# Kernel optimization log

Hardware: AMD Instinct MI355X
Metric: run time of the kernel (lower is better)

Reference implementation:

```python
import jax, jax.numpy as jnp
import numpy as np

OUT_H, OUT_W = 7, 7
SPATIAL_SCALE = 1.0  # aligned=True (align_corners=True interpolate), per init_kwargs


def setup_inputs() -> dict:
    key = jax.random.key(0)
    kf, kb, kx, ky, kw, kh = jax.random.split(key, 6)
    B, C, H, W = 4, 256, 200, 200
    N = 512
    features = jax.random.normal(kf, (B, C, H, W), dtype=jnp.float32)
    batch_idx = jax.random.randint(kb, (N,), 0, B, dtype=jnp.int32)
    # integer boxes with x2>x1, y2>y1, strictly inside the map
    x1 = jax.random.randint(kx, (N,), 0, W - 64, dtype=jnp.int32)
    y1 = jax.random.randint(ky, (N,), 0, H - 64, dtype=jnp.int32)
    bw = jax.random.randint(kw, (N,), 8, 64, dtype=jnp.int32)
    bh = jax.random.randint(kh, (N,), 8, 64, dtype=jnp.int32)
    x2 = jnp.minimum(x1 + bw, W - 1)
    y2 = jnp.minimum(y1 + bh, H - 1)
    rois = jnp.stack([batch_idx, x1, y1, x2, y2], axis=1)  # [N, 5] int32
    return {"features": features, "rois": rois}


def reference(features, rois):
    # features: [B, C, H, W]; rois: [N, 5] int32 (batch, x1, y1, x2, y2)
    # Faithful to: crop features[b, :, y1:y2+1, x1:x2+1] then
    # F.interpolate(size=(7,7), mode='bilinear', align_corners=True).
    N = rois.shape[0]
    H, W = features.shape[2], features.shape[3]
    b = rois[:, 0]
    coords = rois[:, 1:5].astype(jnp.float32) * SPATIAL_SCALE
    x1, y1, x2, y2 = coords[:, 0], coords[:, 1], coords[:, 2], coords[:, 3]

    # align_corners=True source coords inside the crop, offset into the full map
    jy = jnp.arange(OUT_H, dtype=jnp.float32)
    jx = jnp.arange(OUT_W, dtype=jnp.float32)
    sy = y1[:, None] + jy[None, :] * (y2 - y1)[:, None] / (OUT_H - 1)  # [N, OH]
    sx = x1[:, None] + jx[None, :] * (x2 - x1)[:, None] / (OUT_W - 1)  # [N, OW]

    y0f = jnp.floor(sy); x0f = jnp.floor(sx)
    wy = sy - y0f                                  # [N, OH]
    wx = sx - x0f                                  # [N, OW]
    y0 = jnp.clip(y0f.astype(jnp.int32), 0, H - 1)
    y1i = jnp.clip(y0 + 1, 0, H - 1)
    x0 = jnp.clip(x0f.astype(jnp.int32), 0, W - 1)
    x1i = jnp.clip(x0 + 1, 0, W - 1)

    bb = b[:, None, None]                          # [N,1,1]

    def gather(yi, xi):
        # advanced indexing -> [N, OH, OW, C]
        return features[bb, :, yi[:, :, None], xi[:, None, :]]

    v00 = gather(y0, x0)
    v01 = gather(y0, x1i)
    v10 = gather(y1i, x0)
    v11 = gather(y1i, x1i)

    wyb = wy[:, :, None, None]                     # [N, OH, 1, 1]
    wxb = wx[:, None, :, None]                     # [N, 1, OW, 1]
    out = (v00 * (1 - wyb) * (1 - wxb) + v01 * (1 - wyb) * wxb
           + v10 * wyb * (1 - wxb) + v11 * wyb * wxb)  # [N, OH, OW, C]
    return jnp.transpose(out, (0, 3, 1, 2))        # [N, C, OH, OW]
```

## Files before the change

kernel.cpp:

```cpp
#include <hip/hip_runtime.h>
#include <hip/hip_bf16.h>
#include <string.h>

#define OUT_H 7
#define OUT_W 7
#define FEAT_H 200
#define FEAT_W 200
#define HW_ALL (FEAT_H * FEAT_W)
#define HWB  32
#define LSTR 260

__device__ inline unsigned pack2_bf16(float a, float b) {
    __hip_bfloat16 ha = __float2bfloat16(a);
    __hip_bfloat16 hb = __float2bfloat16(b);
    unsigned short ua, ub;
    memcpy(&ua, &ha, 2);
    memcpy(&ub, &hb, 2);
    return (unsigned)ua | ((unsigned)ub << 16);
}

__global__ __launch_bounds__(256) void nchw_to_nhwc_bf16_v2(
    const float* __restrict__ in,
    unsigned*    __restrict__ outu,
    int HW)
{
    __shared__ float tile[HWB * LSTR];
    int hw0 = blockIdx.x * HWB;
    int b   = blockIdx.y;
    const float* inb = in + (size_t)b * 256 * HW + hw0;

    int lane = threadIdx.x & 63;
    int w    = threadIdx.x >> 6;
    int cg   = lane >> 3;
    int xq   = lane & 7;
    int hwr  = xq << 2;

#pragma unroll
    for (int cc = 0; cc < 8; ++cc) {
        int c = (w << 6) + (cc << 3) + cg;
        float4 v = *(const float4*)(inb + (size_t)c * HW + hwr);
        tile[(hwr + 0) * LSTR + c] = v.x;
        tile[(hwr + 1) * LSTR + c] = v.y;
        tile[(hwr + 2) * LSTR + c] = v.z;
        tile[(hwr + 3) * LSTR + c] = v.w;
    }
    __syncthreads();

    uint2* ob = (uint2*)outu + ((size_t)b * HW + hw0) * 64;
    int t = threadIdx.x;
#pragma unroll
    for (int i = 0; i < 8; ++i) {
        int q2  = (i << 8) + t;
        int hr  = q2 >> 6;
        int c0  = (q2 & 63) << 2;
        float4 v = *(const float4*)&tile[hr * LSTR + c0];
        uint2 o;
        o.x = pack2_bf16(v.x, v.y);
        o.y = pack2_bf16(v.z, v.w);
        ob[q2] = o;
    }
}

__global__ __launch_bounds__(256) void roialign_nhwc_v3(
    const uint2* __restrict__ featT2,
    const int*   __restrict__ rois,
    float*       __restrict__ out)
{
    __shared__ float acc[128 * OUT_H * OUT_W];
    const int H = FEAT_H, W = FEAT_W;
    int n = blockIdx.x >> 1;
    int h = blockIdx.x & 1;
    const int* r = rois + n * 5;
    int   b   = r[0];
    float x1f = (float)r[1];
    float y1f = (float)r[2];
    float dx  = (float)r[3] - x1f;
    float dy  = (float)r[4] - y1f;

    int t  = threadIdx.x;
    int pg = t >> 5;
    int cq = t & 31;
    const uint2* fb = featT2 + (size_t)b * HW_ALL * 64 + (h << 5) + cq;

#define BFLO(u) __uint_as_float((u) << 16)
#define BFHI(u) __uint_as_float((u) & 0xffff0000u)

#pragma unroll
    for (int pi = 0; pi < 7; ++pi) {
        int p = (pi << 3) + pg;
        if (p < 49) {
            int jy = p / 7, jx = p % 7;
            float sy = y1f + ((float)jy * dy) / 6.0f;
            float sx = x1f + ((float)jx * dx) / 6.0f;
            float y0fl = floorf(sy), x0fl = floorf(sx);
            float wy = sy - y0fl,    wx = sx - x0fl;
            int y0  = min(max((int)y0fl, 0), H - 1);
            int y1i = min(y0 + 1, H - 1);
            int x0  = min(max((int)x0fl, 0), W - 1);
            int x1i = min(x0 + 1, W - 1);
            float omwy = 1.0f - wy, omwx = 1.0f - wx;
            float w00 = omwy * omwx, w01 = omwy * wx;
            float w10 = wy * omwx,   w11 = wy * wx;

            const uint2* row0 = fb + (size_t)(y0  * W) * 64;
            const uint2* row1 = fb + (size_t)(y1i * W) * 64;
            uint2 u00 = row0[(size_t)x0  * 64];
            uint2 u01 = row0[(size_t)x1i * 64];
            uint2 u10 = row1[(size_t)x0  * 64];
            uint2 u11 = row1[(size_t)x1i * 64];

            float r0 = BFLO(u00.x)*w00 + BFLO(u01.x)*w01 + BFLO(u10.x)*w10 + BFLO(u11.x)*w11;
            float r1 = BFHI(u00.x)*w00 + BFHI(u01.x)*w01 + BFHI(u10.x)*w10 + BFHI(u11.x)*w11;
            float r2 = BFLO(u00.y)*w00 + BFLO(u01.y)*w01 + BFLO(u10.y)*w10 + BFLO(u11.y)*w11;
            float r3 = BFHI(u00.y)*w00 + BFHI(u01.y)*w01 + BFHI(u10.y)*w10 + BFHI(u11.y)*w11;

            int c0 = cq << 2;
            acc[(c0 + 0) * 49 + p] = r0;
            acc[(c0 + 1) * 49 + p] = r1;
            acc[(c0 + 2) * 49 + p] = r2;
            acc[(c0 + 3) * 49 + p] = r3;
        }
    }
    __syncthreads();

    float* ob = out + (size_t)n * (256 * OUT_H * OUT_W) + (size_t)h * (128 * OUT_H * OUT_W);
    const int total = 128 * OUT_H * OUT_W;
    for (int k = t; k < total; k += 256)
        ob[k] = acc[k];
}

__global__ __launch_bounds__(256) void roialign_direct(
    const float* __restrict__ feat, const int* __restrict__ rois,
    float* __restrict__ out, int C, int total)
{
    int idx = blockIdx.x * blockDim.x + threadIdx.x;
    if (idx >= total) return;
    const int H = FEAT_H, W = FEAT_W;
    int jx = idx % OUT_W;
    int t  = idx / OUT_W;
    int jy = t % OUT_H;
    t /= OUT_H;
    int c = t % C;
    int n = t / C;
    const int* r = rois + n * 5;
    int b = r[0];
    float x1 = (float)r[1], y1 = (float)r[2];
    float x2 = (float)r[3], y2 = (float)r[4];
    float sy = y1 + ((float)jy * (y2 - y1)) / (float)(OUT_H - 1);
    float sx = x1 + ((float)jx * (x2 - x1)) / (float)(OUT_W - 1);
    float y0f = floorf(sy), x0f = floorf(sx);
    float wy = sy - y0f, wx = sx - x0f;
    int y0  = min(max((int)y0f, 0), H - 1);
    int y1i = min(y0 + 1, H - 1);
    int x0  = min(max((int)x0f, 0), W - 1);
    int x1i = min(x0 + 1, W - 1);
    const float* fp = feat + ((size_t)b * C + c) * (size_t)(H * W);
    float v00 = fp[y0  * W + x0 ];
    float v01 = fp[y0  * W + x1i];
    float v10 = fp[y1i * W + x0 ];
    float v11 = fp[y1i * W + x1i];
    float omwy = 1.0f - wy, omwx = 1.0f - wx;
    out[idx] = v00 * omwy * omwx + v01 * omwy * wx
             + v10 * wy   * omwx + v11 * wy   * wx;
}

extern "C" void kernel_launch(void* const* d_in, const int* in_sizes, int n_in,
                              void* d_out, int out_size, void* d_ws, size_t ws_size,
                              hipStream_t stream)
{
    const float* feat = (const float*)d_in[0];
    const int*   rois = (const int*)d_in[1];
    float*       out  = (float*)d_out;

    int N  = in_sizes[1] / 5;
    int C  = out_size / (N * OUT_H * OUT_W);
    int HW = FEAT_H * FEAT_W;
    int B  = in_sizes[0] / (C * HW);

    size_t need = (size_t)B * HW * C * sizeof(__hip_bfloat16);
    if (C == 256 && (HW % HWB) == 0 && ws_size >= need) {
        unsigned* featT = (unsigned*)d_ws;
        dim3 tgrid(HW / HWB, B, 1);
        nchw_to_nhwc_bf16_v2<<<tgrid, 256, 0, stream>>>(feat, featT, HW);
        roialign_nhwc_v3<<<N * 2, 256, 0, stream>>>((const uint2*)featT, rois, out);
    } else {
        int total = out_size;
        roialign_direct<<<(total + 255) / 256, 256, 0, stream>>>(feat, rois, out, C, total);
    }
}
```

Measured before the change: 260.2 us.

## Convert features to channel-blocked bf16 layout and split ROIs into four channel groups

The transpose kernel now writes a [B][4 channel groups][HW][64ch] bf16 layout using 160-pixel tiles per 64-channel group, instead of full 256-channel NHWC. Each ROI is handled by four blocks, one per 64-channel group. Each bilinear corner fetch therefore reads a contiguous 128-byte segment within a smaller per-group plane, which should improve locality and raise the number of blocks. The cost is more blocks, each recomputing the ROI coordinates, and a different shared-memory transpose pattern that may cause bank conflicts.

Result: no change. 257.1 us (-1.2%).

```diff
diff --git a/kernel.cpp b/kernel.cpp
--- a/kernel.cpp
+++ b/kernel.cpp
@@ -7,8 +7,8 @@
 #define FEAT_H 200
 #define FEAT_W 200
 #define HW_ALL (FEAT_H * FEAT_W)
-#define HWB  32
-#define LSTR 260
+#define THW 160
+#define TLS 161
 
 __device__ inline unsigned pack2_bf16(float a, float b) {
     __hip_bfloat16 ha = __float2bfloat16(a);
@@ -19,57 +19,55 @@
     return (unsigned)ua | ((unsigned)ub << 16);
 }
 
-__global__ __launch_bounds__(256) void nchw_to_nhwc_bf16_v2(
-    const float* __restrict__ in,
-    unsigned*    __restrict__ outu,
+__global__ __launch_bounds__(256) void nchw_to_blocked_v4(
+    const float* __restrict__ feat,
+    uint2*       __restrict__ featT,
     int HW)
 {
-    __shared__ float tile[HWB * LSTR];
-    int hw0 = blockIdx.x * HWB;
-    int b   = blockIdx.y;
-    const float* inb = in + (size_t)b * 256 * HW + hw0;
-
-    int lane = threadIdx.x & 63;
-    int w    = threadIdx.x >> 6;
-    int cg   = lane >> 3;
-    int xq   = lane & 7;
-    int hwr  = xq << 2;
+    __shared__ float tile[64 * TLS];
+    int hw0 = blockIdx.x * THW;
+    int cg  = blockIdx.y;
+    int b   = blockIdx.z;
+    const float* src = feat + ((size_t)b * 256 + cg * 64) * HW + hw0;
+    int t = threadIdx.x;
 
 #pragma unroll
-    for (int cc = 0; cc < 8; ++cc) {
-        int c = (w << 6) + (cc << 3) + cg;
-        float4 v = *(const float4*)(inb + (size_t)c * HW + hwr);
-        tile[(hwr + 0) * LSTR + c] = v.x;
-        tile[(hwr + 1) * LSTR + c] = v.y;
-        tile[(hwr + 2) * LSTR + c] = v.z;
-        tile[(hwr + 3) * LSTR + c] = v.w;
+    for (int i = 0; i < 10; ++i) {
+        int flat = i * 256 + t;
+        int c = flat / 40;
+        int q = flat % 40;
+        float4 v = *(const float4*)(src + (size_t)c * HW + q * 4);
+        float* d = &tile[c * TLS + q * 4];
+        d[0] = v.x; d[1] = v.y; d[2] = v.z; d[3] = v.w;
     }
     __syncthreads();
 
-    uint2* ob = (uint2*)outu + ((size_t)b * HW + hw0) * 64;
-    int t = threadIdx.x;
+    uint2* dst = featT + ((size_t)(b * 4 + cg) * HW + hw0) * 16;
 #pragma unroll
-    for (int i = 0; i < 8; ++i) {
-        int q2  = (i << 8) + t;
-        int hr  = q2 >> 6;
-        int c0  = (q2 & 63) << 2;
-        float4 v = *(const float4*)&tile[hr * LSTR + c0];
-        uint2 o;
-        o.x = pack2_bf16(v.x, v.y);
-        o.y = pack2_bf16(v.z, v.w);
-        ob[q2] = o;
+    for (int i = 0; i < 10; ++i) {
+        int o  = i * 256 + t;
+        int hw = o >> 4;
+        int cq = o & 15;
+        float a0 = tile[(cq * 4 + 0) * TLS + hw];
+        float a1 = tile[(cq * 4 + 1) * TLS + hw];
+        float a2 = tile[(cq * 4 + 2) * TLS + hw];
+        float a3 = tile[(cq * 4 + 3) * TLS + hw];
+        uint2 u;
+        u.x = pack2_bf16(a0, a1);
+        u.y = pack2_bf16(a2, a3);
+        dst[o] = u;
     }
 }
 
-__global__ __launch_bounds__(256) void roialign_nhwc_v3(
-    const uint2* __restrict__ featT2,
+__global__ __launch_bounds__(256) void roialign_blocked_v4(
+    const uint2* __restrict__ featT,
     const int*   __restrict__ rois,
     float*       __restrict__ out)
 {
-    __shared__ float acc[128 * OUT_H * OUT_W];
+    __shared__ float acc[64 * OUT_H * OUT_W];
     const int H = FEAT_H, W = FEAT_W;
-    int n = blockIdx.x >> 1;
-    int h = blockIdx.x & 1;
+    int n  = blockIdx.x >> 2;
+    int cg = blockIdx.x & 3;
     const int* r = rois + n * 5;
     int   b   = r[0];
     float x1f = (float)r[1];
@@ -78,16 +76,16 @@
     float dy  = (float)r[4] - y1f;
 
     int t  = threadIdx.x;
-    int pg = t >> 5;
-    int cq = t & 31;
-    const uint2* fb = featT2 + (size_t)b * HW_ALL * 64 + (h << 5) + cq;
+    int cq = t & 15;
+    int pg = t >> 4;
+    const uint2* fb = featT + ((size_t)(b * 4 + cg) * HW_ALL) * 16 + cq;
 
 #define BFLO(u) __uint_as_float((u) << 16)
 #define BFHI(u) __uint_as_float((u) & 0xffff0000u)
 
 #pragma unroll
-    for (int pi = 0; pi < 7; ++pi) {
-        int p = (pi << 3) + pg;
+    for (int pi = 0; pi < 4; ++pi) {
+        int p = (pi << 4) + pg;
         if (p < 49) {
             int jy = p / 7, jx = p % 7;
             float sy = y1f + ((float)jy * dy) / 6.0f;
@@ -102,12 +100,10 @@
             float w00 = omwy * omwx, w01 = omwy * wx;
             float w10 = wy * omwx,   w11 = wy * wx;
 
-            const uint2* row0 = fb + (size_t)(y0  * W) * 64;
-            const uint2* row1 = fb + (size_t)(y1i * W) * 64;
-            uint2 u00 = row0[(size_t)x0  * 64];
-            uint2 u01 = row0[(size_t)x1i * 64];
-            uint2 u10 = row1[(size_t)x0  * 64];
-            uint2 u11 = row1[(size_t)x1i * 64];
+            uint2 u00 = fb[(size_t)(y0  * W + x0 ) * 16];
+            uint2 u01 = fb[(size_t)(y0  * W + x1i) * 16];
+            uint2 u10 = fb[(size_t)(y1i * W + x0 ) * 16];
+            uint2 u11 = fb[(size_t)(y1i * W + x1i) * 16];
 
             float r0 = BFLO(u00.x)*w00 + BFLO(u01.x)*w01 + BFLO(u10.x)*w10 + BFLO(u11.x)*w11;
             float r1 = BFHI(u00.x)*w00 + BFHI(u01.x)*w01 + BFHI(u10.x)*w10 + BFHI(u11.x)*w11;
@@ -123,19 +119,18 @@
     }
     __syncthreads();
 
-    float* ob = out + (size_t)n * (256 * OUT_H * OUT_W) + (size_t)h * (128 * OUT_H * OUT_W);
-    const int total = 128 * OUT_H * OUT_W;
+    float* ob = out + ((size_t)n * 256 + cg * 64) * (OUT_H * OUT_W);
+    const int total = 64 * OUT_H * OUT_W;
     for (int k = t; k < total; k += 256)
         ob[k] = acc[k];
 }
 
 __global__ __launch_bounds__(256) void roialign_direct(
     const float* __restrict__ feat, const int* __restrict__ rois,
-    float* __restrict__ out, int C, int total)
+    float* __restrict__ out, int C, int H, int W, int total)
 {
     int idx = blockIdx.x * blockDim.x + threadIdx.x;
     if (idx >= total) return;
-    const int H = FEAT_H, W = FEAT_W;
     int jx = idx % OUT_W;
     int t  = idx / OUT_W;
     int jy = t % OUT_H;
@@ -174,17 +169,17 @@
 
     int N  = in_sizes[1] / 5;
     int C  = out_size / (N * OUT_H * OUT_W);
-    int HW = FEAT_H * FEAT_W;
-    int B  = in_sizes[0] / (C * HW);
+    int B  = in_sizes[0] / (C * HW_ALL);
 
-    size_t need = (size_t)B * HW * C * sizeof(__hip_bfloat16);
-    if (C == 256 && (HW % HWB) == 0 && ws_size >= need) {
-        unsigned* featT = (unsigned*)d_ws;
-        dim3 tgrid(HW / HWB, B, 1);
-        nchw_to_nhwc_bf16_v2<<<tgrid, 256, 0, stream>>>(feat, featT, HW);
-        roialign_nhwc_v3<<<N * 2, 256, 0, stream>>>((const uint2*)featT, rois, out);
+    size_t need = (size_t)B * HW_ALL * 256 * sizeof(__hip_bfloat16);
+    if (C == 256 && in_sizes[0] == B * 256 * HW_ALL && ws_size >= need) {
+        uint2* featT = (uint2*)d_ws;
+        dim3 tgrid(HW_ALL / THW, 4, B);
+        nchw_to_blocked_v4<<<tgrid, 256, 0, stream>>>(feat, featT, HW_ALL);
+        roialign_blocked_v4<<<N * 4, 256, 0, stream>>>(featT, rois, out);
     } else {
         int total = out_size;
-        roialign_direct<<<(total + 255) / 256, 256, 0, stream>>>(feat, rois, out, C, total);
+        roialign_direct<<<(total + 255) / 256, 256, 0, stream>>>(
+            feat, rois, out, C, FEAT_H, FEAT_W, total);
     }
 }
```
